# Kernel optimization log

Measured on AMD Instinct MI355X. Metric: run time of the kernel, lower is better.

The kernel has to match this reference:

```python
import jax, jax.numpy as jnp
import numpy as np

N_NODES = 100000


def gcn_conv(x, src, dst, norm, W, b):
    # PyG GCNConv: linear transform first, then normalized scatter-add aggregation, then bias.
    xw = x @ W                                   # [N, out]
    msgs = xw[src] * norm[:, None]               # [E+N, out] gathered, degree-normalized messages
    out = jax.ops.segment_sum(msgs, dst, num_segments=N_NODES)
    return out + b


def _build_graph(edge_index):
    # add self-loops (PyG gcn_norm default)
    loop = jnp.arange(N_NODES, dtype=edge_index.dtype)
    src = jnp.concatenate([edge_index[0], loop])
    dst = jnp.concatenate([edge_index[1], loop])
    deg = jax.ops.segment_sum(jnp.ones_like(dst, dtype=jnp.float32), dst, num_segments=N_NODES)
    dis = jnp.where(deg > 0, jax.lax.rsqrt(jnp.maximum(deg, 1.0)), 0.0)
    norm = dis[src] * dis[dst]                   # D^-1/2 (A+I) D^-1/2 edge weights
    return src, dst, norm


def setup_inputs() -> dict:
    key = jax.random.key(0)
    ks = jax.random.split(key, 6)
    F_IN, H, C, E = 128, 128, 8, 1600000
    x = jax.random.normal(ks[0], (N_NODES, F_IN), dtype=jnp.float32)
    edge_index = jax.random.randint(ks[1], (2, E), 0, N_NODES, dtype=jnp.int64)
    # glorot-style init for conv weights
    W1 = jax.random.normal(ks[2], (F_IN, H), dtype=jnp.float32) * (1.0 / np.sqrt(F_IN))
    b1 = jnp.zeros((H,), dtype=jnp.float32)
    W2 = jax.random.normal(ks[3], (H, C), dtype=jnp.float32) * (1.0 / np.sqrt(H))
    b2 = jnp.zeros((C,), dtype=jnp.float32)
    return {"x": x, "edge_index": edge_index, "W1": W1, "b1": b1, "W2": W2, "b2": b2}


def reference(x, edge_index, W1, b1, W2, b2):
    src, dst, norm = _build_graph(edge_index)
    h = gcn_conv(x, src, dst, norm, W1, b1)
    h = jax.nn.relu(h)
    # dropout is identity in eval mode
    out = gcn_conv(h, src, dst, norm, W2, b2)
    return jax.nn.log_softmax(out, axis=1)
```

## Files before the change

### kernel.cpp

```cpp
#include <hip/hip_runtime.h>

#define N_NODES 100000
#define NBKT 782
#define EPB 8192
#define SL_STRIDE 800000

typedef unsigned int uint;
typedef __attribute__((ext_vector_type(8))) short bf16x8;
typedef __attribute__((ext_vector_type(4))) float f32x4;

union FragU { uint4 u; bf16x8 b; };

__device__ __forceinline__ uint pack_bf16_2(float a, float b) {
    uint ua = __float_as_uint(a), ub = __float_as_uint(b);
    ua += 0x7fff + ((ua >> 16) & 1);
    ub += 0x7fff + ((ub >> 16) & 1);
    return (ua >> 16) | (ub & 0xffff0000u);
}
__device__ __forceinline__ float bf_lo(uint u) { return __uint_as_float(u << 16); }
__device__ __forceinline__ float bf_hi(uint u) { return __uint_as_float(u & 0xffff0000u); }

__device__ __forceinline__ int edge_at(const int* __restrict__ ei, int idx, int is64) {
    return is64 ? ei[2 * idx] : ei[idx];
}

__device__ __forceinline__ int block_probe_is64(const int* __restrict__ ei, int* sh) {
    int t = threadIdx.x;
    if (t == 0) *sh = 0;
    __syncthreads();
    int any = 0;
    for (int j = t; j < 4096; j += blockDim.x) any |= ei[2 * j + 1];
    if (any) atomicOr(sh, 1);
    __syncthreads();
    return (*sh == 0);
}

__global__ __launch_bounds__(256) void kA1(const int* __restrict__ ei, int E,
                                           int* __restrict__ slab) {
    __shared__ int h[NBKT];
    __shared__ int shp;
    int t = threadIdx.x;
    int is64 = block_probe_is64(ei, &shp);
    for (int i = t; i < NBKT; i += 256) h[i] = 0;
    __syncthreads();
    int base = blockIdx.x * EPB;
    int end = min(base + EPB, E);
    for (int e = base + t; e < end; e += 256) {
        int d = edge_at(ei, E + e, is64);
        atomicAdd(&h[d >> 7], 1);
    }
    __syncthreads();
    for (int i = t; i < NBKT; i += 256)
        slab[(size_t)blockIdx.x * NBKT + i] = h[i];
}

__global__ __launch_bounds__(256) void kA2a(const int* __restrict__ slab, int PB,
                                            int* __restrict__ bkt_cnt) {
    int w = threadIdx.x >> 6;
    int l = threadIdx.x & 63;
    int k = blockIdx.x * 4 + w;
    if (k >= NBKT) return;
    int v = 0;
    for (int b = l; b < PB; b += 64)
        v += slab[(size_t)b * NBKT + k];
#pragma unroll
    for (int s = 32; s; s >>= 1) v += __shfl_xor(v, s, 64);
    if (l == 0) bkt_cnt[k] = v;
}

__global__ __launch_bounds__(1024) void kA2b(const int* __restrict__ bkt_cnt,
                                             int* __restrict__ bkt_off,
                                             int* __restrict__ bkt_cursor) {
    __shared__ int s[1024];
    int t = threadIdx.x;
    int v = (t < NBKT) ? bkt_cnt[t] : 0;
    s[t] = v;
    __syncthreads();
    for (int d = 1; d < 1024; d <<= 1) {
        int y = (t >= d) ? s[t - d] : 0;
        __syncthreads();
        s[t] += y;
        __syncthreads();
    }
    if (t < NBKT) {
        int o = s[t] - v;
        bkt_off[t] = o;
        bkt_cursor[t] = o;
    }
}

__global__ __launch_bounds__(256) void kA3(const int* __restrict__ ei, int E,
                                           int* __restrict__ bkt_cursor,
                                           uint* __restrict__ bkt_data) {
    __shared__ int h[NBKT];
    __shared__ int base[NBKT];
    __shared__ int shp;
    int t = threadIdx.x;
    int is64 = block_probe_is64(ei, &shp);
    for (int i = t; i < NBKT; i += 256) h[i] = 0;
    __syncthreads();
    int lo = blockIdx.x * EPB;
    int end = min(lo + EPB, E);
    for (int e = lo + t; e < end; e += 256) {
        int d = edge_at(ei, E + e, is64);
        atomicAdd(&h[d >> 7], 1);
    }
    __syncthreads();
    for (int i = t; i < NBKT; i += 256) {
        int c = h[i];
        base[i] = c ? atomicAdd(&bkt_cursor[i], c) : 0;
    }
    __syncthreads();
    for (int i = t; i < NBKT; i += 256) h[i] = 0;
    __syncthreads();
    for (int e = lo + t; e < end; e += 256) {
        int d = edge_at(ei, E + e, is64);
        int s = edge_at(ei, e, is64);
        int b = d >> 7;
        int r = atomicAdd(&h[b], 1);
        bkt_data[base[b] + r] = ((uint)s << 7) | (uint)(d & 127);
    }
}

__global__ __launch_bounds__(256) void kB(const uint* __restrict__ bkt_data,
                                          const int* __restrict__ bkt_off,
                                          const int* __restrict__ bkt_cnt,
                                          int* __restrict__ srcs,
                                          int* __restrict__ count,
                                          int* __restrict__ offs,
                                          float* __restrict__ dis,
                                          float* __restrict__ y2) {
    __shared__ int lc[128];
    __shared__ int sc[128];
    __shared__ int lcur[128];
    int t = threadIdx.x;
    int b = blockIdx.x;
    {
        int zb = b * 1024;
        int ze = min(zb + 1024, N_NODES * 8);
        for (int i = zb + t; i < ze; i += 256) y2[i] = 0.0f;
    }
    if (t < 128) { lc[t] = 0; lcur[t] = 0; }
    __syncthreads();
    int start = bkt_off[b];
    int n = bkt_cnt[b];
    for (int i = t; i < n; i += 256)
        atomicAdd(&lc[bkt_data[start + i] & 127], 1);
    __syncthreads();
    if (t < 128) sc[t] = lc[t];
    __syncthreads();
    for (int d = 1; d < 128; d <<= 1) {
        int y = 0;
        if (t < 128 && t >= d) y = sc[t - d];
        __syncthreads();
        if (t < 128) sc[t] += y;
        __syncthreads();
    }
    if (t < 128) {
        int node = b * 128 + t;
        if (node < N_NODES) {
            int c = lc[t];
            count[node] = c;
            offs[node] = start + sc[t] - c;
            dis[node] = rsqrtf((float)c + 1.0f);
        }
    }
    __syncthreads();
    for (int i = t; i < n; i += 256) {
        uint rec = bkt_data[start + i];
        int dl = rec & 127;
        int r = atomicAdd(&lcur[dl], 1);
        srcs[start + (sc[dl] - lc[dl]) + r] = rec >> 7;
    }
}

__global__ __launch_bounds__(256) void k_gemm1(const float* __restrict__ x,
                                               const float* __restrict__ W,
                                               const float* __restrict__ dis,
                                               uint* __restrict__ y1s) {
    __shared__ uint4 WtA[2048];
    char* wt = (char*)WtA;
    int t = threadIdx.x;

    const float4* W4 = (const float4*)W;
#pragma unroll
    for (int ii = 0; ii < 4; ++ii) {
        int tile = t + 256 * ii;
        int nq = tile >> 5, kq = tile & 31;
        float4 r0 = W4[(4 * kq + 0) * 32 + nq];
        float4 r1 = W4[(4 * kq + 1) * 32 + nq];
        float4 r2 = W4[(4 * kq + 2) * 32 + nq];
        float4 r3 = W4[(4 * kq + 3) * 32 + nq];
        const float* p0 = (const float*)&r0;
        const float* p1 = (const float*)&r1;
        const float* p2 = (const float*)&r2;
        const float* p3 = (const float*)&r3;
#pragma unroll
        for (int cc = 0; cc < 4; ++cc) {
            int n = 4 * nq + cc;
            uint2 v;
            v.x = pack_bf16_2(p0[cc], p1[cc]);
            v.y = pack_bf16_2(p2[cc], p3[cc]);
            *(uint2*)(wt + n * 256 + (((kq >> 1) ^ (n & 7)) << 4) + ((kq & 1) << 3)) = v;
        }
    }
    __syncthreads();

    int w = t >> 6, lane = t & 63;
    int m = lane & 15, kg = lane >> 4;
    int row0 = blockIdx.x * 64 + 16 * w;

    int arow = row0 + m;
    bool av = arow < N_NODES;
    const float4* xr = (const float4*)(x + (size_t)arow * 128);
    float4 z4 = make_float4(0.f, 0.f, 0.f, 0.f);
    FragU af[4];
#pragma unroll
    for (int kf = 0; kf < 4; ++kf) {
        float4 g0 = av ? xr[8 * kf + 2 * kg]     : z4;
        float4 g1 = av ? xr[8 * kf + 2 * kg + 1] : z4;
        const float* a0 = (const float*)&g0;
        const float* a1 = (const float*)&g1;
        af[kf].u.x = pack_bf16_2(a0[0], a0[1]);
        af[kf].u.y = pack_bf16_2(a0[2], a0[3]);
        af[kf].u.z = pack_bf16_2(a1[0], a1[1]);
        af[kf].u.w = pack_bf16_2(a1[2], a1[3]);
    }

    int crow = row0 + 4 * kg;
    float dd[4];
#pragma unroll
    for (int rr = 0; rr < 4; ++rr)
        dd[rr] = (crow + rr < N_NODES) ? dis[crow + rr] : 0.0f;

#pragma unroll
    for (int ct = 0; ct < 8; ++ct) {
        f32x4 acc = {0.f, 0.f, 0.f, 0.f};
#pragma unroll
        for (int kf = 0; kf < 4; ++kf) {
            int n = 16 * ct + m;
            bf16x8 bw = *(const bf16x8*)(wt + n * 256 + ((((kf << 2) | kg) ^ (n & 7)) << 4));
            acc = __builtin_amdgcn_mfma_f32_16x16x32_bf16(af[kf].b, bw, acc, 0, 0, 0);
        }
#pragma unroll
        for (int rr = 0; rr < 4; ++rr) {
            float v = acc[rr] * dd[rr];
            float p = __shfl_xor(v, 1, 64);
            if (!(lane & 1)) {
                int grow = crow + rr;
                if (grow < N_NODES)
                    y1s[(size_t)ct * SL_STRIDE + grow * 8 + (m >> 1)] = pack_bf16_2(v, p);
            }
        }
    }
}

__global__ __launch_bounds__(256) void k_agg1s(const uint* __restrict__ y1s,
                                               const int* __restrict__ srcs,
                                               const int* __restrict__ offs,
                                               const int* __restrict__ count,
                                               const float* __restrict__ dis,
                                               const float* __restrict__ b1,
                                               const float* __restrict__ W2,
                                               float* __restrict__ y2) {
    int t = threadIdx.x;
    int slice = blockIdx.x & 7;
    int nb = blockIdx.x >> 3;
    int g = t >> 3;
    int j = t & 7;
    int d = nb * 32 + g;

    float w0[8], w1[8];
    const float* wr0 = W2 + (size_t)(slice * 16 + 2 * j) * 8;
#pragma unroll
    for (int c = 0; c < 8; ++c) { w0[c] = wr0[c]; w1[c] = wr0[8 + c]; }

    const uint4* ybase = (const uint4*)(y1s + (size_t)slice * SL_STRIDE);
    float acc[16];
#pragma unroll
    for (int c = 0; c < 16; ++c) acc[c] = 0.0f;

    int st = offs[d], n = count[d];
    for (int i = j; i <= n; i += 8) {
        int sk = d;
        if (i < n) sk = srcs[st + i];
        uint4 a  = ybase[(size_t)sk * 2];
        uint4 bq = ybase[(size_t)sk * 2 + 1];
        acc[0]  += bf_lo(a.x);  acc[1]  += bf_hi(a.x);
        acc[2]  += bf_lo(a.y);  acc[3]  += bf_hi(a.y);
        acc[4]  += bf_lo(a.z);  acc[5]  += bf_hi(a.z);
        acc[6]  += bf_lo(a.w);  acc[7]  += bf_hi(a.w);
        acc[8]  += bf_lo(bq.x); acc[9]  += bf_hi(bq.x);
        acc[10] += bf_lo(bq.y); acc[11] += bf_hi(bq.y);
        acc[12] += bf_lo(bq.z); acc[13] += bf_hi(bq.z);
        acc[14] += bf_lo(bq.w); acc[15] += bf_hi(bq.w);
    }

    int hi4 = (j >> 2) & 1, hi2 = (j >> 1) & 1, hi1 = j & 1;
    float v8[8];
#pragma unroll
    for (int c = 0; c < 8; ++c) {
        float keep = hi4 ? acc[c + 8] : acc[c];
        float send = hi4 ? acc[c] : acc[c + 8];
        v8[c] = keep + __shfl_xor(send, 4, 8);
    }
    float v4[4];
#pragma unroll
    for (int c = 0; c < 4; ++c) {
        float keep = hi2 ? v8[c + 4] : v8[c];
        float send = hi2 ? v8[c] : v8[c + 4];
        v4[c] = keep + __shfl_xor(send, 2, 8);
    }
    float v2[2];
#pragma unroll
    for (int c = 0; c < 2; ++c) {
        float keep = hi1 ? v4[c + 2] : v4[c];
        float send = hi1 ? v4[c] : v4[c + 2];
        v2[c] = keep + __shfl_xor(send, 1, 8);
    }

    float ddv = dis[d];
    float2 b = ((const float2*)b1)[slice * 8 + j];
    float h0 = fmaxf(fmaf(v2[0], ddv, b.x), 0.0f);
    float h1 = fmaxf(fmaf(v2[1], ddv, b.y), 0.0f);

    float p[8];
#pragma unroll
    for (int c = 0; c < 8; ++c) p[c] = h0 * w0[c] + h1 * w1[c];
    float q4[4];
#pragma unroll
    for (int c = 0; c < 4; ++c) {
        float keep = hi4 ? p[c + 4] : p[c];
        float send = hi4 ? p[c] : p[c + 4];
        q4[c] = keep + __shfl_xor(send, 4, 8);
    }
    float q2[2];
#pragma unroll
    for (int c = 0; c < 2; ++c) {
        float keep = hi2 ? q4[c + 2] : q4[c];
        float send = hi2 ? q4[c] : q4[c + 2];
        q2[c] = keep + __shfl_xor(send, 2, 8);
    }
    float keep = hi1 ? q2[1] : q2[0];
    float send = hi1 ? q2[0] : q2[1];
    float q = keep + __shfl_xor(send, 1, 8);

    atomicAdd(&y2[(size_t)d * 8 + j], q * ddv);
}

__global__ __launch_bounds__(256) void k_agg2(const float* __restrict__ y2,
                                              const int* __restrict__ srcs,
                                              const int* __restrict__ offs,
                                              const int* __restrict__ count,
                                              const float* __restrict__ dis,
                                              const float* __restrict__ b2,
                                              float* __restrict__ out) {
    int g = (blockIdx.x * 256 + threadIdx.x) >> 3;
    int c = threadIdx.x & 7;
    if (g >= N_NODES) return;
    float acc = y2[(size_t)g * 8 + c];
    float acc2 = 0.0f;
    int st = offs[g], n = count[g];
    int i = 0;
    for (; i + 2 <= n; i += 2) {
        int s0 = srcs[st + i], s1 = srcs[st + i + 1];
        acc  += y2[(size_t)s0 * 8 + c];
        acc2 += y2[(size_t)s1 * 8 + c];
    }
    if (i < n) acc += y2[(size_t)srcs[st + i] * 8 + c];
    acc += acc2;

    float o = fmaf(acc, dis[g], b2[c]);
    float m = o;
#pragma unroll
    for (int k = 1; k < 8; k <<= 1) m = fmaxf(m, __shfl_xor(m, k, 64));
    float e = expf(o - m);
    float ssum = e;
#pragma unroll
    for (int k = 1; k < 8; k <<= 1) ssum += __shfl_xor(ssum, k, 64);
    out[(size_t)g * 8 + c] = (o - m) - logf(ssum);
}

extern "C" void kernel_launch(void* const* d_in, const int* in_sizes, int n_in,
                              void* d_out, int out_size, void* d_ws, size_t ws_size,
                              hipStream_t stream) {
    const float* x  = (const float*)d_in[0];
    const int*   ei = (const int*)d_in[1];
    const float* W1 = (const float*)d_in[2];
    const float* b1 = (const float*)d_in[3];
    const float* W2 = (const float*)d_in[4];
    const float* b2 = (const float*)d_in[5];
    float* out = (float*)d_out;
    const int E = in_sizes[1] / 2;
    const int PB = (E + EPB - 1) / EPB;
    const int Epad = (E + 3) & ~3;
    int slabInts = (PB * NBKT + 3) & ~3;

    int*   slab       = (int*)d_ws;
    int*   bkt_cnt    = slab + slabInts;
    int*   bkt_off    = bkt_cnt + 784;
    int*   bkt_cursor = bkt_off + 784;
    int*   count      = bkt_cursor + 784;
    int*   offs       = count + N_NODES;
    float* dis        = (float*)(offs + N_NODES);
    uint*  bkt_data   = (uint*)(dis + N_NODES);
    int*   srcs       = (int*)(bkt_data + Epad);
    uint*  y1s        = (uint*)(srcs + Epad);
    float* y2         = (float*)(y1s + (size_t)8 * SL_STRIDE);

    kA1    <<<PB, 256, 0, stream>>>(ei, E, slab);
    kA2a   <<<(NBKT + 3) / 4, 256, 0, stream>>>(slab, PB, bkt_cnt);
    kA2b   <<<1, 1024, 0, stream>>>(bkt_cnt, bkt_off, bkt_cursor);
    kA3    <<<PB, 256, 0, stream>>>(ei, E, bkt_cursor, bkt_data);
    kB     <<<NBKT, 256, 0, stream>>>(bkt_data, bkt_off, bkt_cnt, srcs, count, offs, dis, y2);

    k_gemm1<<<(N_NODES + 63) / 64, 256, 0, stream>>>(x, W1, dis, y1s);
    k_agg1s<<<8 * 3125, 256, 0, stream>>>(y1s, srcs, offs, count, dis, b1, W2, y2);
    k_agg2 <<<(N_NODES + 31) / 32, 256, 0, stream>>>(y2, srcs, offs, count, dis, b2, out);
}
```

Measured before the change: 222.2 us.

## Widen aggregation slices to 32 features and precompute per-block bucket offsets

The first-layer aggregation now uses 4 feature slices of 32 bf16 values (64 bytes per node) instead of 8 slices of 16, which halves the number of times the edge list and index arrays are reread. The cost is 32 accumulators per thread and fewer blocks. The bucket scatter now takes exclusive per-block offsets from a column scan done in kA2a. This removes kA3's duplicate histogram pass, its global atomics on bucket cursors and its re-probe of the index width, which is now passed through a flag written by kA1.

```diff
diff --git a/kernel.cpp b/kernel.cpp
--- a/kernel.cpp
+++ b/kernel.cpp
@@ -3,7 +3,8 @@
 #define N_NODES 100000
 #define NBKT 782
 #define EPB 8192
-#define SL_STRIDE 800000
+#define NSL 4
+#define SL2 1600000
 
 typedef unsigned int uint;
 typedef __attribute__((ext_vector_type(8))) short bf16x8;
@@ -36,11 +37,13 @@
 }
 
 __global__ __launch_bounds__(256) void kA1(const int* __restrict__ ei, int E,
-                                           int* __restrict__ slab) {
+                                           int* __restrict__ slab,
+                                           int* __restrict__ gflag) {
     __shared__ int h[NBKT];
     __shared__ int shp;
     int t = threadIdx.x;
     int is64 = block_probe_is64(ei, &shp);
+    if (blockIdx.x == 0 && t == 0) gflag[0] = is64 ? 0 : 1;
     for (int i = t; i < NBKT; i += 256) h[i] = 0;
     __syncthreads();
     int base = blockIdx.x * EPB;
@@ -54,23 +57,30 @@
         slab[(size_t)blockIdx.x * NBKT + i] = h[i];
 }
 
-__global__ __launch_bounds__(256) void kA2a(const int* __restrict__ slab, int PB,
+__global__ __launch_bounds__(256) void kA2a(int* __restrict__ slab, int PB,
                                             int* __restrict__ bkt_cnt) {
     int w = threadIdx.x >> 6;
     int l = threadIdx.x & 63;
     int k = blockIdx.x * 4 + w;
     if (k >= NBKT) return;
-    int v = 0;
-    for (int b = l; b < PB; b += 64)
-        v += slab[(size_t)b * NBKT + k];
-#pragma unroll
-    for (int s = 32; s; s >>= 1) v += __shfl_xor(v, s, 64);
-    if (l == 0) bkt_cnt[k] = v;
+    int carry = 0;
+    for (int base = 0; base < PB; base += 64) {
+        int row = base + l;
+        int v = (row < PB) ? slab[(size_t)row * NBKT + k] : 0;
+        int incl = v;
+#pragma unroll
+        for (int d = 1; d < 64; d <<= 1) {
+            int y = __shfl_up(incl, d, 64);
+            if (l >= d) incl += y;
+        }
+        if (row < PB) slab[(size_t)row * NBKT + k] = carry + incl - v;
+        carry += __shfl(incl, 63, 64);
+    }
+    if (l == 0) bkt_cnt[k] = carry;
 }
 
 __global__ __launch_bounds__(1024) void kA2b(const int* __restrict__ bkt_cnt,
-                                             int* __restrict__ bkt_off,
-                                             int* __restrict__ bkt_cursor) {
+                                             int* __restrict__ bkt_off) {
     __shared__ int s[1024];
     int t = threadIdx.x;
     int v = (t < NBKT) ? bkt_cnt[t] : 0;
@@ -82,43 +92,31 @@
         s[t] += y;
         __syncthreads();
     }
-    if (t < NBKT) {
-        int o = s[t] - v;
-        bkt_off[t] = o;
-        bkt_cursor[t] = o;
-    }
+    if (t < NBKT) bkt_off[t] = s[t] - v;
 }
 
 __global__ __launch_bounds__(256) void kA3(const int* __restrict__ ei, int E,
-                                           int* __restrict__ bkt_cursor,
+                                           const int* __restrict__ gflag,
+                                           const int* __restrict__ slab,
+                                           const int* __restrict__ bkt_off,
                                            uint* __restrict__ bkt_data) {
     __shared__ int h[NBKT];
-    __shared__ int base[NBKT];
-    __shared__ int shp;
-    int t = threadIdx.x;
-    int is64 = block_probe_is64(ei, &shp);
-    for (int i = t; i < NBKT; i += 256) h[i] = 0;
+    __shared__ int pre[NBKT];
+    int t = threadIdx.x;
+    int is64 = (gflag[0] == 0);
+    for (int i = t; i < NBKT; i += 256) {
+        h[i] = 0;
+        pre[i] = bkt_off[i] + slab[(size_t)blockIdx.x * NBKT + i];
+    }
     __syncthreads();
     int lo = blockIdx.x * EPB;
     int end = min(lo + EPB, E);
-    for (int e = lo + t; e < end; e += 256) {
-        int d = edge_at(ei, E + e, is64);
-        atomicAdd(&h[d >> 7], 1);
-    }
-    __syncthreads();
-    for (int i = t; i < NBKT; i += 256) {
-        int c = h[i];
-        base[i] = c ? atomicAdd(&bkt_cursor[i], c) : 0;
-    }
-    __syncthreads();
-    for (int i = t; i < NBKT; i += 256) h[i] = 0;
-    __syncthreads();
     for (int e = lo + t; e < end; e += 256) {
         int d = edge_at(ei, E + e, is64);
         int s = edge_at(ei, e, is64);
         int b = d >> 7;
         int r = atomicAdd(&h[b], 1);
-        bkt_data[base[b] + r] = ((uint)s << 7) | (uint)(d & 127);
+        bkt_data[pre[b] + r] = ((uint)s << 7) | (uint)(d & 127);
     }
 }
 
@@ -249,7 +247,8 @@
             if (!(lane & 1)) {
                 int grow = crow + rr;
                 if (grow < N_NODES)
-                    y1s[(size_t)ct * SL_STRIDE + grow * 8 + (m >> 1)] = pack_bf16_2(v, p);
+                    y1s[(size_t)(ct >> 1) * SL2 + grow * 16 + (ct & 1) * 8 + (m >> 1)]
+                        = pack_bf16_2(v, p);
             }
         }
     }
@@ -264,69 +263,78 @@
                                                const float* __restrict__ W2,
                                                float* __restrict__ y2) {
     int t = threadIdx.x;
-    int slice = blockIdx.x & 7;
-    int nb = blockIdx.x >> 3;
+    int slice = blockIdx.x & 3;
+    int nb = blockIdx.x >> 2;
     int g = t >> 3;
     int j = t & 7;
     int d = nb * 32 + g;
 
-    float w0[8], w1[8];
-    const float* wr0 = W2 + (size_t)(slice * 16 + 2 * j) * 8;
-#pragma unroll
-    for (int c = 0; c < 8; ++c) { w0[c] = wr0[c]; w1[c] = wr0[8 + c]; }
-
-    const uint4* ybase = (const uint4*)(y1s + (size_t)slice * SL_STRIDE);
-    float acc[16];
-#pragma unroll
-    for (int c = 0; c < 16; ++c) acc[c] = 0.0f;
+    const uint4* ybase = (const uint4*)(y1s + (size_t)slice * SL2);
+    float acc[32];
+#pragma unroll
+    for (int c = 0; c < 32; ++c) acc[c] = 0.0f;
 
     int st = offs[d], n = count[d];
     for (int i = j; i <= n; i += 8) {
         int sk = d;
         if (i < n) sk = srcs[st + i];
-        uint4 a  = ybase[(size_t)sk * 2];
-        uint4 bq = ybase[(size_t)sk * 2 + 1];
-        acc[0]  += bf_lo(a.x);  acc[1]  += bf_hi(a.x);
-        acc[2]  += bf_lo(a.y);  acc[3]  += bf_hi(a.y);
-        acc[4]  += bf_lo(a.z);  acc[5]  += bf_hi(a.z);
-        acc[6]  += bf_lo(a.w);  acc[7]  += bf_hi(a.w);
-        acc[8]  += bf_lo(bq.x); acc[9]  += bf_hi(bq.x);
-        acc[10] += bf_lo(bq.y); acc[11] += bf_hi(bq.y);
-        acc[12] += bf_lo(bq.z); acc[13] += bf_hi(bq.z);
-        acc[14] += bf_lo(bq.w); acc[15] += bf_hi(bq.w);
+        uint4 q0 = ybase[(size_t)sk * 4];
+        uint4 q1 = ybase[(size_t)sk * 4 + 1];
+        uint4 q2 = ybase[(size_t)sk * 4 + 2];
+        uint4 q3 = ybase[(size_t)sk * 4 + 3];
+        acc[0]  += bf_lo(q0.x); acc[1]  += bf_hi(q0.x);
+        acc[2]  += bf_lo(q0.y); acc[3]  += bf_hi(q0.y);
+        acc[4]  += bf_lo(q0.z); acc[5]  += bf_hi(q0.z);
+        acc[6]  += bf_lo(q0.w); acc[7]  += bf_hi(q0.w);
+        acc[8]  += bf_lo(q1.x); acc[9]  += bf_hi(q1.x);
+        acc[10] += bf_lo(q1.y); acc[11] += bf_hi(q1.y);
+        acc[12] += bf_lo(q1.z); acc[13] += bf_hi(q1.z);
+        acc[14] += bf_lo(q1.w); acc[15] += bf_hi(q1.w);
+        acc[16] += bf_lo(q2.x); acc[17] += bf_hi(q2.x);
+        acc[18] += bf_lo(q2.y); acc[19] += bf_hi(q2.y);
+        acc[20] += bf_lo(q2.z); acc[21] += bf_hi(q2.z);
+        acc[22] += bf_lo(q2.w); acc[23] += bf_hi(q2.w);
+        acc[24] += bf_lo(q3.x); acc[25] += bf_hi(q3.x);
+        acc[26] += bf_lo(q3.y); acc[27] += bf_hi(q3.y);
+        acc[28] += bf_lo(q3.z); acc[29] += bf_hi(q3.z);
+        acc[30] += bf_lo(q3.w); acc[31] += bf_hi(q3.w);
     }
 
     int hi4 = (j >> 2) & 1, hi2 = (j >> 1) & 1, hi1 = j & 1;
+    float v16[16];
+#pragma unroll
+    for (int c = 0; c < 16; ++c) {
+        float keep = hi4 ? acc[c + 16] : acc[c];
+        float send = hi4 ? acc[c] : acc[c + 16];
+        v16[c] = keep + __shfl_xor(send, 4, 8);
+    }
     float v8[8];
 #pragma unroll
     for (int c = 0; c < 8; ++c) {
-        float keep = hi4 ? acc[c + 8] : acc[c];
-        float send = hi4 ? acc[c] : acc[c + 8];
-        v8[c] = keep + __shfl_xor(send, 4, 8);
+        float keep = hi2 ? v16[c + 8] : v16[c];
+        float send = hi2 ? v16[c] : v16[c + 8];
+        v8[c] = keep + __shfl_xor(send, 2, 8);
     }
     float v4[4];
 #pragma unroll
     for (int c = 0; c < 4; ++c) {
-        float keep = hi2 ? v8[c + 4] : v8[c];
-        float send = hi2 ? v8[c] : v8[c + 4];
-        v4[c] = keep + __shfl_xor(send, 2, 8);
-    }
-    float v2[2];
-#pragma unroll
-    for (int c = 0; c < 2; ++c) {
-        float keep = hi1 ? v4[c + 2] : v4[c];
-        float send = hi1 ? v4[c] : v4[c + 2];
-        v2[c] = keep + __shfl_xor(send, 1, 8);
+        float keep = hi1 ? v8[c + 4] : v8[c];
+        float send = hi1 ? v8[c] : v8[c + 4];
+        v4[c] = keep + __shfl_xor(send, 1, 8);
     }
 
     float ddv = dis[d];
-    float2 b = ((const float2*)b1)[slice * 8 + j];
-    float h0 = fmaxf(fmaf(v2[0], ddv, b.x), 0.0f);
-    float h1 = fmaxf(fmaf(v2[1], ddv, b.y), 0.0f);
-
+    float4 bv = ((const float4*)b1)[slice * 8 + j];
+    float h0 = fmaxf(fmaf(v4[0], ddv, bv.x), 0.0f);
+    float h1 = fmaxf(fmaf(v4[1], ddv, bv.y), 0.0f);
+    float h2 = fmaxf(fmaf(v4[2], ddv, bv.z), 0.0f);
+    float h3 = fmaxf(fmaf(v4[3], ddv, bv.w), 0.0f);
+
+    const float* wr = W2 + (size_t)(slice * 32 + 4 * j) * 8;
     float p[8];
 #pragma unroll
-    for (int c = 0; c < 8; ++c) p[c] = h0 * w0[c] + h1 * w1[c];
+    for (int c = 0; c < 8; ++c)
+        p[c] = h0 * wr[c] + h1 * wr[8 + c] + h2 * wr[16 + c] + h3 * wr[24 + c];
     float q4[4];
 #pragma unroll
     for (int c = 0; c < 4; ++c) {
@@ -396,25 +404,25 @@
     const int Epad = (E + 3) & ~3;
     int slabInts = (PB * NBKT + 3) & ~3;
 
-    int*   slab       = (int*)d_ws;
-    int*   bkt_cnt    = slab + slabInts;
-    int*   bkt_off    = bkt_cnt + 784;
-    int*   bkt_cursor = bkt_off + 784;
-    int*   count      = bkt_cursor + 784;
-    int*   offs       = count + N_NODES;
-    float* dis        = (float*)(offs + N_NODES);
-    uint*  bkt_data   = (uint*)(dis + N_NODES);
-    int*   srcs       = (int*)(bkt_data + Epad);
-    uint*  y1s        = (uint*)(srcs + Epad);
-    float* y2         = (float*)(y1s + (size_t)8 * SL_STRIDE);
-
-    kA1    <<<PB, 256, 0, stream>>>(ei, E, slab);
+    int*   slab     = (int*)d_ws;
+    int*   bkt_cnt  = slab + slabInts;
+    int*   bkt_off  = bkt_cnt + 784;
+    int*   gflag    = bkt_off + 784;
+    int*   count    = gflag + 4;
+    int*   offs     = count + N_NODES;
+    float* dis      = (float*)(offs + N_NODES);
+    uint*  bkt_data = (uint*)(dis + N_NODES);
+    int*   srcs     = (int*)(bkt_data + Epad);
+    uint*  y1s      = (uint*)(srcs + Epad);
+    float* y2       = (float*)(y1s + (size_t)NSL * SL2);
+
+    kA1    <<<PB, 256, 0, stream>>>(ei, E, slab, gflag);
     kA2a   <<<(NBKT + 3) / 4, 256, 0, stream>>>(slab, PB, bkt_cnt);
-    kA2b   <<<1, 1024, 0, stream>>>(bkt_cnt, bkt_off, bkt_cursor);
-    kA3    <<<PB, 256, 0, stream>>>(ei, E, bkt_cursor, bkt_data);
+    kA2b   <<<1, 1024, 0, stream>>>(bkt_cnt, bkt_off);
+    kA3    <<<PB, 256, 0, stream>>>(ei, E, gflag, slab, bkt_off, bkt_data);
     kB     <<<NBKT, 256, 0, stream>>>(bkt_data, bkt_off, bkt_cnt, srcs, count, offs, dis, y2);
 
     k_gemm1<<<(N_NODES + 63) / 64, 256, 0, stream>>>(x, W1, dis, y1s);
-    k_agg1s<<<8 * 3125, 256, 0, stream>>>(y1s, srcs, offs, count, dis, b1, W2, y2);
+    k_agg1s<<<NSL * 3125, 256, 0, stream>>>(y1s, srcs, offs, count, dis, b1, W2, y2);
     k_agg2 <<<(N_NODES + 31) / 32, 256, 0, stream>>>(y2, srcs, offs, count, dis, b2, out);
 }
```

New measurement: 233.0 us. +4.9%, slower.

## Precompute per-block bucket offsets via scan and parallelize second aggregation over edges

Applied to the files above, without the earlier changes.

The bucket-count slab is now scanned per bucket across partition blocks, giving each block its exact write offset. kA3 no longer recounts its edges, does no global atomic cursor reservation and skips the int64 probe, reading a flag written by kA1 instead. The final aggregation splits each node's neighbor list across 8 lanes, each loading full 8-float rows, and combines them with a shuffle transpose-reduce. This removes a redundant pass over the edge array and improves load parallelism, at the cost of a slightly more complex scan and a cross-kernel flag dependency.

```diff
diff --git a/kernel.cpp b/kernel.cpp
--- a/kernel.cpp
+++ b/kernel.cpp
@@ -36,11 +36,13 @@
 }
 
 __global__ __launch_bounds__(256) void kA1(const int* __restrict__ ei, int E,
-                                           int* __restrict__ slab) {
+                                           int* __restrict__ slab,
+                                           int* __restrict__ gflag) {
     __shared__ int h[NBKT];
     __shared__ int shp;
     int t = threadIdx.x;
     int is64 = block_probe_is64(ei, &shp);
+    if (blockIdx.x == 0 && t == 0) gflag[0] = is64 ? 0 : 1;
     for (int i = t; i < NBKT; i += 256) h[i] = 0;
     __syncthreads();
     int base = blockIdx.x * EPB;
@@ -54,23 +56,30 @@
         slab[(size_t)blockIdx.x * NBKT + i] = h[i];
 }
 
-__global__ __launch_bounds__(256) void kA2a(const int* __restrict__ slab, int PB,
+__global__ __launch_bounds__(256) void kA2a(int* __restrict__ slab, int PB,
                                             int* __restrict__ bkt_cnt) {
     int w = threadIdx.x >> 6;
     int l = threadIdx.x & 63;
     int k = blockIdx.x * 4 + w;
     if (k >= NBKT) return;
-    int v = 0;
-    for (int b = l; b < PB; b += 64)
-        v += slab[(size_t)b * NBKT + k];
-#pragma unroll
-    for (int s = 32; s; s >>= 1) v += __shfl_xor(v, s, 64);
-    if (l == 0) bkt_cnt[k] = v;
+    int carry = 0;
+    for (int base = 0; base < PB; base += 64) {
+        int row = base + l;
+        int v = (row < PB) ? slab[(size_t)row * NBKT + k] : 0;
+        int incl = v;
+#pragma unroll
+        for (int d = 1; d < 64; d <<= 1) {
+            int y = __shfl_up(incl, d, 64);
+            if (l >= d) incl += y;
+        }
+        if (row < PB) slab[(size_t)row * NBKT + k] = carry + incl - v;
+        carry += __shfl(incl, 63, 64);
+    }
+    if (l == 0) bkt_cnt[k] = carry;
 }
 
 __global__ __launch_bounds__(1024) void kA2b(const int* __restrict__ bkt_cnt,
-                                             int* __restrict__ bkt_off,
-                                             int* __restrict__ bkt_cursor) {
+                                             int* __restrict__ bkt_off) {
     __shared__ int s[1024];
     int t = threadIdx.x;
     int v = (t < NBKT) ? bkt_cnt[t] : 0;
@@ -82,43 +91,31 @@
         s[t] += y;
         __syncthreads();
     }
-    if (t < NBKT) {
-        int o = s[t] - v;
-        bkt_off[t] = o;
-        bkt_cursor[t] = o;
-    }
+    if (t < NBKT) bkt_off[t] = s[t] - v;
 }
 
 __global__ __launch_bounds__(256) void kA3(const int* __restrict__ ei, int E,
-                                           int* __restrict__ bkt_cursor,
+                                           const int* __restrict__ gflag,
+                                           const int* __restrict__ slab,
+                                           const int* __restrict__ bkt_off,
                                            uint* __restrict__ bkt_data) {
     __shared__ int h[NBKT];
-    __shared__ int base[NBKT];
-    __shared__ int shp;
-    int t = threadIdx.x;
-    int is64 = block_probe_is64(ei, &shp);
-    for (int i = t; i < NBKT; i += 256) h[i] = 0;
+    __shared__ int pre[NBKT];
+    int t = threadIdx.x;
+    int is64 = (gflag[0] == 0);
+    for (int i = t; i < NBKT; i += 256) {
+        h[i] = 0;
+        pre[i] = bkt_off[i] + slab[(size_t)blockIdx.x * NBKT + i];
+    }
     __syncthreads();
     int lo = blockIdx.x * EPB;
     int end = min(lo + EPB, E);
-    for (int e = lo + t; e < end; e += 256) {
-        int d = edge_at(ei, E + e, is64);
-        atomicAdd(&h[d >> 7], 1);
-    }
-    __syncthreads();
-    for (int i = t; i < NBKT; i += 256) {
-        int c = h[i];
-        base[i] = c ? atomicAdd(&bkt_cursor[i], c) : 0;
-    }
-    __syncthreads();
-    for (int i = t; i < NBKT; i += 256) h[i] = 0;
-    __syncthreads();
     for (int e = lo + t; e < end; e += 256) {
         int d = edge_at(ei, E + e, is64);
         int s = edge_at(ei, e, is64);
         int b = d >> 7;
         int r = atomicAdd(&h[b], 1);
-        bkt_data[base[b] + r] = ((uint)s << 7) | (uint)(d & 127);
+        bkt_data[pre[b] + r] = ((uint)s << 7) | (uint)(d & 127);
     }
 }
 
@@ -355,22 +352,43 @@
                                               const float* __restrict__ dis,
                                               const float* __restrict__ b2,
                                               float* __restrict__ out) {
-    int g = (blockIdx.x * 256 + threadIdx.x) >> 3;
-    int c = threadIdx.x & 7;
+    int t = threadIdx.x;
+    int g = (blockIdx.x * 256 + t) >> 3;
+    int j = t & 7;
     if (g >= N_NODES) return;
-    float acc = y2[(size_t)g * 8 + c];
-    float acc2 = 0.0f;
+    const float4* yb = (const float4*)y2;
+    float acc[8];
+#pragma unroll
+    for (int c = 0; c < 8; ++c) acc[c] = 0.0f;
     int st = offs[g], n = count[g];
-    int i = 0;
-    for (; i + 2 <= n; i += 2) {
-        int s0 = srcs[st + i], s1 = srcs[st + i + 1];
-        acc  += y2[(size_t)s0 * 8 + c];
-        acc2 += y2[(size_t)s1 * 8 + c];
-    }
-    if (i < n) acc += y2[(size_t)srcs[st + i] * 8 + c];
-    acc += acc2;
-
-    float o = fmaf(acc, dis[g], b2[c]);
+    for (int i = j; i <= n; i += 8) {
+        int sk = g;
+        if (i < n) sk = srcs[st + i];
+        float4 a = yb[(size_t)sk * 2];
+        float4 b = yb[(size_t)sk * 2 + 1];
+        acc[0] += a.x; acc[1] += a.y; acc[2] += a.z; acc[3] += a.w;
+        acc[4] += b.x; acc[5] += b.y; acc[6] += b.z; acc[7] += b.w;
+    }
+    int hi4 = (j >> 2) & 1, hi2 = (j >> 1) & 1, hi1 = j & 1;
+    float v4[4];
+#pragma unroll
+    for (int c = 0; c < 4; ++c) {
+        float keep = hi4 ? acc[c + 4] : acc[c];
+        float send = hi4 ? acc[c] : acc[c + 4];
+        v4[c] = keep + __shfl_xor(send, 4, 8);
+    }
+    float v2[2];
+#pragma unroll
+    for (int c = 0; c < 2; ++c) {
+        float keep = hi2 ? v4[c + 2] : v4[c];
+        float send = hi2 ? v4[c] : v4[c + 2];
+        v2[c] = keep + __shfl_xor(send, 2, 8);
+    }
+    float keep = hi1 ? v2[1] : v2[0];
+    float send = hi1 ? v2[0] : v2[1];
+    float q = keep + __shfl_xor(send, 1, 8);
+
+    float o = fmaf(q, dis[g], b2[j]);
     float m = o;
 #pragma unroll
     for (int k = 1; k < 8; k <<= 1) m = fmaxf(m, __shfl_xor(m, k, 64));
@@ -378,7 +396,7 @@
     float ssum = e;
 #pragma unroll
     for (int k = 1; k < 8; k <<= 1) ssum += __shfl_xor(ssum, k, 64);
-    out[(size_t)g * 8 + c] = (o - m) - logf(ssum);
+    out[(size_t)g * 8 + j] = (o - m) - logf(ssum);
 }
 
 extern "C" void kernel_launch(void* const* d_in, const int* in_sizes, int n_in,
@@ -396,25 +414,25 @@
     const int Epad = (E + 3) & ~3;
     int slabInts = (PB * NBKT + 3) & ~3;
 
-    int*   slab       = (int*)d_ws;
-    int*   bkt_cnt    = slab + slabInts;
-    int*   bkt_off    = bkt_cnt + 784;
-    int*   bkt_cursor = bkt_off + 784;
-    int*   count      = bkt_cursor + 784;
-    int*   offs       = count + N_NODES;
-    float* dis        = (float*)(offs + N_NODES);
-    uint*  bkt_data   = (uint*)(dis + N_NODES);
-    int*   srcs       = (int*)(bkt_data + Epad);
-    uint*  y1s        = (uint*)(srcs + Epad);
-    float* y2         = (float*)(y1s + (size_t)8 * SL_STRIDE);
-
-    kA1    <<<PB, 256, 0, stream>>>(ei, E, slab);
+    int*   slab     = (int*)d_ws;
+    int*   bkt_cnt  = slab + slabInts;
+    int*   bkt_off  = bkt_cnt + 784;
+    int*   gflag    = bkt_off + 784;
+    int*   count    = gflag + 4;
+    int*   offs     = count + N_NODES;
+    float* dis      = (float*)(offs + N_NODES);
+    uint*  bkt_data = (uint*)(dis + N_NODES);
+    int*   srcs     = (int*)(bkt_data + Epad);
+    uint*  y1s      = (uint*)(srcs + Epad);
+    float* y2       = (float*)(y1s + (size_t)8 * SL_STRIDE);
+
+    kA1    <<<PB, 256, 0, stream>>>(ei, E, slab, gflag);
     kA2a   <<<(NBKT + 3) / 4, 256, 0, stream>>>(slab, PB, bkt_cnt);
-    kA2b   <<<1, 1024, 0, stream>>>(bkt_cnt, bkt_off, bkt_cursor);
-    kA3    <<<PB, 256, 0, stream>>>(ei, E, bkt_cursor, bkt_data);
+    kA2b   <<<1, 1024, 0, stream>>>(bkt_cnt, bkt_off);
+    kA3    <<<PB, 256, 0, stream>>>(ei, E, gflag, slab, bkt_off, bkt_data);
     kB     <<<NBKT, 256, 0, stream>>>(bkt_data, bkt_off, bkt_cnt, srcs, count, offs, dis, y2);
 
     k_gemm1<<<(N_NODES + 63) / 64, 256, 0, stream>>>(x, W1, dis, y1s);
     k_agg1s<<<8 * 3125, 256, 0, stream>>>(y1s, srcs, offs, count, dis, b1, W2, y2);
-    k_agg2 <<<(N_NODES + 31) / 32, 256, 0, stream>>>(y2, srcs, offs, count, dis, b2, out);
-}
+    k_agg2 <<<(N_NODES * 8 + 255) / 256, 256, 0, stream>>>(y2, srcs, offs, count, dis, b2, out);
+}
```

Measured after the change: 218.8 us. Within noise of the previous version (-1.5%).
